# Optimization experiments

Measured on AMD Instinct MI355X. Metric: run time of the kernel, lower is better.

The kernel has to match this reference:

```python
import jax, jax.numpy as jnp
import numpy as np

K = 3  # kernel_size

def _bn(x, g, b, m, v, eps=1e-5):
    # inference-mode BatchNorm2d over channel axis 1
    sh = (1, -1, 1, 1)
    return (x - m.reshape(sh)) * (g.reshape(sh) / jnp.sqrt(v.reshape(sh) + eps)) + b.reshape(sh)

def setup_inputs() -> dict:
    key = jax.random.key(0)
    ks = jax.random.split(key, 12)
    B, C, H, W, OC = 8, 128, 96, 96, 256
    k2 = K * K
    x = jax.random.normal(ks[0], (B, C, H, W), jnp.float32)
    # get_weight grouped 1x1 conv: [C*9,1,1,1] stored compactly as [C,9]
    w1 = jax.random.normal(ks[1], (C, k2), jnp.float32) * 0.1
    # generate_feature grouped 3x3 conv (groups=C, multiplier 9): OIHW [C*9,1,3,3]
    gf_w = jax.random.normal(ks[2], (C * k2, 1, K, K), jnp.float32) * 0.1
    bn1_g = jax.random.uniform(ks[3], (C * k2,), jnp.float32, 0.5, 1.5)
    bn1_b = jax.random.normal(ks[4], (C * k2,), jnp.float32) * 0.1
    bn1_m = jax.random.normal(ks[5], (C * k2,), jnp.float32) * 0.1
    bn1_v = jax.random.uniform(ks[6], (C * k2,), jnp.float32, 0.5, 1.5)
    conv_w = jax.random.normal(ks[7], (OC, C, K, K), jnp.float32) * (1.0 / np.sqrt(C * k2))
    conv_b = jax.random.normal(ks[8], (OC,), jnp.float32) * 0.1
    bn2_g = jax.random.uniform(ks[9], (OC,), jnp.float32, 0.5, 1.5)
    bn2_b = jax.random.normal(ks[10], (OC,), jnp.float32) * 0.1
    bn2_m = jax.random.normal(ks[11], (OC,), jnp.float32) * 0.1
    bn2_v = jax.random.uniform(jax.random.fold_in(key, 99), (OC,), jnp.float32, 0.5, 1.5)
    return {"x": x, "w1": w1, "gf_w": gf_w, "bn1_g": bn1_g, "bn1_b": bn1_b,
            "bn1_m": bn1_m, "bn1_v": bn1_v, "conv_w": conv_w, "conv_b": conv_b,
            "bn2_g": bn2_g, "bn2_b": bn2_b, "bn2_m": bn2_m, "bn2_v": bn2_v}

def reference(x, w1, gf_w, bn1_g, bn1_b, bn1_m, bn1_v, conv_w, conv_b, bn2_g, bn2_b, bn2_m, bn2_v):
    B, C, H, W = x.shape
    k2 = K * K
    # --- get_weight: AvgPool2d(k=3, pad=1, stride=1, count_include_pad) + grouped 1x1 conv ---
    pooled = jax.lax.reduce_window(x, 0.0, jax.lax.add, (1, 1, K, K), (1, 1, 1, 1),
                                   [(0, 0), (0, 0), (1, 1), (1, 1)]) / float(k2)
    weight = jnp.einsum('bchw,cn->bcnhw', pooled, w1)  # [B,C,9,H,W]
    attn = jax.nn.softmax(weight, axis=2)
    # --- generate_feature: depthwise 3x3 conv (groups=C, mult 9) + BN + ReLU ---
    feat = jax.lax.conv_general_dilated(x, gf_w, (1, 1), [(1, 1), (1, 1)],
                                        dimension_numbers=('NCHW', 'OIHW', 'NCHW'),
                                        feature_group_count=C)
    feat = jax.nn.relu(_bn(feat, bn1_g, bn1_b, bn1_m, bn1_v)).reshape(B, C, k2, H, W)
    # --- attention reweight + space-to-depth rearrange 'b c (n1 n2) h w -> b c (h n1) (w n2)' ---
    wd = (feat * attn).reshape(B, C, K, K, H, W)
    wd = wd.transpose(0, 1, 4, 2, 5, 3).reshape(B, C, H * K, W * K)
    # --- final conv k=3 stride=3 + BN + ReLU ---
    out = jax.lax.conv_general_dilated(wd, conv_w, (K, K), [(0, 0), (0, 0)],
                                       dimension_numbers=('NCHW', 'OIHW', 'NCHW'))
    out = out + conv_b.reshape(1, -1, 1, 1)
    return jax.nn.relu(_bn(out, bn2_g, bn2_b, bn2_m, bn2_v))
```

## Files before the change

### kernel.cpp

```cpp
#include <hip/hip_runtime.h>
#include <hip/hip_bf16.h>


#define CCH  128
#define OCN  256
#define HH   96
#define WWD  96
#define KCH  1152
#define PIMG 9216
#define BNP  64
#define NBLK 144
#define CC   32
#define KC   288
#define VP   296
#define NT   512

using short8  = __attribute__((ext_vector_type(8))) short;
using f32x4   = __attribute__((ext_vector_type(4))) float;
using f32x2   = __attribute__((ext_vector_type(2))) float;

__device__ __forceinline__ ushort bf16bits(float f) {
    __hip_bfloat16 h = __float2bfloat16(f);
    return *reinterpret_cast<ushort*>(&h);
}

struct NB { f32x2 p[4]; float s; };

__global__ void prep_kernel(const float* __restrict__ W2, const float* __restrict__ gfw,
                            const float* __restrict__ bn1g, const float* __restrict__ bn1b,
                            const float* __restrict__ bn1m, const float* __restrict__ bn1v,
                            const float* __restrict__ w1,
                            ushort* __restrict__ W2bf, float* __restrict__ gws,
                            float* __restrict__ shiftv, float* __restrict__ w1s) {
    int i = blockIdx.x * 256 + threadIdx.x;
    if (i < OCN * KCH) {
        W2bf[i] = bf16bits(W2[i]);
    } else if (i < OCN * KCH + KCH) {
        const int ch = i - OCN * KCH;
        const float sc = bn1g[ch] * rsqrtf(bn1v[ch] + 1e-5f);
        shiftv[ch] = bn1b[ch] - bn1m[ch] * sc;
        #pragma unroll
        for (int t = 0; t < 9; ++t) gws[ch * 12 + t] = gfw[ch * 9 + t] * sc;
    } else if (i < OCN * KCH + KCH + CCH) {
        const int c = i - OCN * KCH - KCH;
        #pragma unroll
        for (int n = 0; n < 9; ++n) w1s[c * 12 + n] = w1[c * 9 + n] * (1.f / 9.f);
    }
}

__device__ __forceinline__ NB load_nb(const float* __restrict__ xc,
                                      const int hro0, const int hro1, const int hro2,
                                      const int wx0, const int wx1, const int wx2) {
    NB r;
    float v0 = xc[hro0 + wx0], v1 = xc[hro0 + wx1], v2 = xc[hro0 + wx2];
    float v3 = xc[hro1 + wx0], v4 = xc[hro1 + wx1], v5 = xc[hro1 + wx2];
    float v6 = xc[hro2 + wx0], v7 = xc[hro2 + wx1], v8 = xc[hro2 + wx2];
    r.p[0] = f32x2{v0, v1}; r.p[1] = f32x2{v2, v3};
    r.p[2] = f32x2{v4, v5}; r.p[3] = f32x2{v6, v7};
    r.s = v8;
    return r;
}

template<bool FAST>
__global__ __launch_bounds__(NT, 4) void rfa_mfma3_kernel(
    const float* __restrict__ x,
    const float* __restrict__ w1,   const float* __restrict__ gfw,
    const float* __restrict__ bn1g, const float* __restrict__ bn1b,
    const float* __restrict__ bn1m, const float* __restrict__ bn1v,
    const float* __restrict__ W2f,
    const ushort* __restrict__ W2bf, const float* __restrict__ gws,
    const float* __restrict__ shiftv, const float* __restrict__ w1s,
    const float* __restrict__ cbias,
    const float* __restrict__ bn2g, const float* __restrict__ bn2b,
    const float* __restrict__ bn2m, const float* __restrict__ bn2v,
    float* __restrict__ out)
{
    __shared__ ushort vlds[2][BNP * VP];

    const int tid = threadIdx.x;
    const int b   = blockIdx.x / NBLK;
    const int P0  = (blockIdx.x % NBLK) * BNP;

    const int px  = tid & 63;
    const int p   = P0 + px;
    const int h   = p / WWD;
    const int w   = p - h * WWD;
    const int wid = __builtin_amdgcn_readfirstlane(tid >> 6);
    const int l15 = px & 15;
    const int lhi = px >> 4;

    int hro[3], wxc[3];
    f32x2 okp[4];
    float ok8;
    {
        float okr[3], okc[3];
        #pragma unroll
        for (int d = 0; d < 3; ++d) {
            int hy = h + d - 1;
            okr[d] = ((unsigned)hy < (unsigned)HH) ? 1.f : 0.f;
            hro[d] = ((hy < 0) ? 0 : (hy > 95 ? 95 : hy)) * WWD;
            int wx = w + d - 1;
            okc[d] = ((unsigned)wx < (unsigned)WWD) ? 1.f : 0.f;
            wxc[d] = (wx < 0) ? 0 : (wx > 95 ? 95 : wx);
        }
        float o[9];
        #pragma unroll
        for (int dy = 0; dy < 3; ++dy)
            #pragma unroll
            for (int dx = 0; dx < 3; ++dx) o[dy*3+dx] = okr[dy] * okc[dx];
        okp[0] = f32x2{o[0], o[1]}; okp[1] = f32x2{o[2], o[3]};
        okp[2] = f32x2{o[4], o[5]}; okp[3] = f32x2{o[6], o[7]};
        ok8 = o[8];
    }

    f32x4 acc[2][4] = {};
    const float* xb = x + (size_t)b * CCH * PIMG;
    const int abase = (wid * 32 + l15) * KCH + lhi * 8;

    auto chan = [&](int q) { return (q >> 2) * CC + wid * 4 + (q & 3); };

    NB nb = load_nb(xb + (size_t)chan(0) * PIMG, hro[0], hro[1], hro[2], wxc[0], wxc[1], wxc[2]);

    for (int ck = 0; ck < 4; ++ck) {
        ushort* vbuf = vlds[ck & 1];

        #pragma unroll
        for (int pass = 0; pass < 4; ++pass) {
            const int q  = ck * 4 + pass;
            const int qn = (q + 1 > 15) ? 15 : q + 1;
            NB nbn = load_nb(xb + (size_t)chan(qn) * PIMG,
                             hro[0], hro[1], hro[2], wxc[0], wxc[1], wxc[2]);

            const int c  = chan(q);
            const int cl = wid * 4 + pass;
            f32x2 e[4];
            #pragma unroll
            for (int i = 0; i < 4; ++i) e[i] = nb.p[i] * okp[i];
            const float e8 = nb.s * ok8;
            f32x2 ps2 = (e[0] + e[1]) + (e[2] + e[3]);
            const float psum = ps2[0] + ps2[1] + e8;

            float at[9], ss = 0.f;
            if constexpr (FAST) {
                const float* w1r = w1s + c * 12;
                #pragma unroll
                for (int n = 0; n < 9; ++n) { at[n] = __expf(psum * w1r[n]); ss += at[n]; }
            } else {
                const float pooled = psum * (1.f / 9.f);
                const float* w1r = w1 + c * 9;
                #pragma unroll
                for (int n = 0; n < 9; ++n) { at[n] = __expf(pooled * w1r[n]); ss += at[n]; }
            }
            const float rs = __builtin_amdgcn_rcpf(ss);

            ushort* vp = vbuf + px * VP + cl * 9;
            #pragma unroll
            for (int n = 0; n < 9; ++n) {
                const int ch = c * 9 + n;
                float f;
                if constexpr (FAST) {
                    const f32x2* gp = reinterpret_cast<const f32x2*>(gws + ch * 12);
                    f32x2 f2 = f32x2{shiftv[ch], 0.f};
                    #pragma unroll
                    for (int t = 0; t < 4; ++t) f2 = __builtin_elementwise_fma(e[t], gp[t], f2);
                    f = f2[0] + f2[1];
                    f = fmaf(e8, gws[ch * 12 + 8], f);
                } else {
                    const float* gr = gfw + ch * 9;
                    float cv = 0.f;
                    cv = fmaf(e[0][0], gr[0], cv); cv = fmaf(e[0][1], gr[1], cv);
                    cv = fmaf(e[1][0], gr[2], cv); cv = fmaf(e[1][1], gr[3], cv);
                    cv = fmaf(e[2][0], gr[4], cv); cv = fmaf(e[2][1], gr[5], cv);
                    cv = fmaf(e[3][0], gr[6], cv); cv = fmaf(e[3][1], gr[7], cv);
                    cv = fmaf(e8, gr[8], cv);
                    const float sc = bn1g[ch] * rsqrtf(bn1v[ch] + 1e-5f);
                    f = (cv - bn1m[ch]) * sc + bn1b[ch];
                }
                f = fmaxf(f, 0.f) * (at[n] * rs);
                vp[n] = bf16bits(f);
            }
            nb = nbn;
        }
        __syncthreads();

        const int k0 = ck * KC;
        #pragma unroll 3
        for (int kk = 0; kk < 9; ++kk) {
            short8 afr[2], bfr[4];
            #pragma unroll
            for (int mi = 0; mi < 2; ++mi) {
                const int ai = abase + mi * 16 * KCH + k0 + kk * 32;
                if constexpr (FAST) {
                    afr[mi] = *reinterpret_cast<const short8*>(W2bf + ai);
                } else {
                    const f32x4 f0 = *reinterpret_cast<const f32x4*>(W2f + ai);
                    const f32x4 f1 = *reinterpret_cast<const f32x4*>(W2f + ai + 4);
                    short8 a;
                    a[0] = (short)bf16bits(f0[0]); a[1] = (short)bf16bits(f0[1]);
                    a[2] = (short)bf16bits(f0[2]); a[3] = (short)bf16bits(f0[3]);
                    a[4] = (short)bf16bits(f1[0]); a[5] = (short)bf16bits(f1[1]);
                    a[6] = (short)bf16bits(f1[2]); a[7] = (short)bf16bits(f1[3]);
                    afr[mi] = a;
                }
            }
            #pragma unroll
            for (int ni = 0; ni < 4; ++ni) {
                const ushort* bp = vbuf + (ni * 16 + l15) * VP + kk * 32 + lhi * 8;
                bfr[ni] = *reinterpret_cast<const short8*>(bp);
            }
            #pragma unroll
            for (int mi = 0; mi < 2; ++mi)
                #pragma unroll
                for (int ni = 0; ni < 4; ++ni)
                    acc[mi][ni] = __builtin_amdgcn_mfma_f32_16x16x32_bf16(
                        afr[mi], bfr[ni], acc[mi][ni], 0, 0, 0);
        }
    }

    #pragma unroll
    for (int mi = 0; mi < 2; ++mi) {
        #pragma unroll
        for (int r = 0; r < 4; ++r) {
            const int oc = wid * 32 + mi * 16 + lhi * 4 + r;
            const float s2 = bn2g[oc] * rsqrtf(bn2v[oc] + 1e-5f);
            const float t2 = (cbias[oc] - bn2m[oc]) * s2 + bn2b[oc];
            float* op = out + ((size_t)(b * OCN + oc)) * PIMG + P0;
            #pragma unroll
            for (int ni = 0; ni < 4; ++ni)
                op[ni * 16 + l15] = fmaxf(fmaf(acc[mi][ni][r], s2, t2), 0.f);
        }
    }
}

extern "C" void kernel_launch(void* const* d_in, const int* in_sizes, int n_in,
                              void* d_out, int out_size, void* d_ws, size_t ws_size,
                              hipStream_t stream) {
    const float* xx   = (const float*)d_in[0];
    const float* w1   = (const float*)d_in[1];
    const float* gfw  = (const float*)d_in[2];
    const float* bn1g = (const float*)d_in[3];
    const float* bn1b = (const float*)d_in[4];
    const float* bn1m = (const float*)d_in[5];
    const float* bn1v = (const float*)d_in[6];
    const float* W2   = (const float*)d_in[7];
    const float* cb   = (const float*)d_in[8];
    const float* bn2g = (const float*)d_in[9];
    const float* bn2b = (const float*)d_in[10];
    const float* bn2m = (const float*)d_in[11];
    const float* bn2v = (const float*)d_in[12];
    float* o = (float*)d_out;

    const size_t off_gws   = (size_t)OCN * KCH * sizeof(ushort);
    const size_t off_shift = off_gws + (size_t)KCH * 12 * sizeof(float);
    const size_t off_w1s   = off_shift + (size_t)KCH * sizeof(float);
    const size_t ws_need   = off_w1s + (size_t)CCH * 12 * sizeof(float);

    dim3 grid(8 * NBLK);
    dim3 blk(NT);

    if (ws_size >= ws_need) {
        ushort* W2bf = (ushort*)d_ws;
        float*  gwsp = (float*)((char*)d_ws + off_gws);
        float*  shf  = (float*)((char*)d_ws + off_shift);
        float*  w1sp = (float*)((char*)d_ws + off_w1s);
        const int ptot = OCN * KCH + KCH + CCH;
        prep_kernel<<<(ptot + 255) / 256, 256, 0, stream>>>(
            W2, gfw, bn1g, bn1b, bn1m, bn1v, w1, W2bf, gwsp, shf, w1sp);
        rfa_mfma3_kernel<true><<<grid, blk, 0, stream>>>(
            xx, w1, gfw, bn1g, bn1b, bn1m, bn1v, W2, W2bf, gwsp, shf, w1sp,
            cb, bn2g, bn2b, bn2m, bn2v, o);
    } else {
        rfa_mfma3_kernel<false><<<grid, blk, 0, stream>>>(
            xx, w1, gfw, bn1g, bn1b, bn1m, bn1v, W2, nullptr, nullptr, nullptr, nullptr,
            cb, bn2g, bn2b, bn2m, bn2v, o);
    }
}
```

Measured before the change: 210.4 us.

## Halve pixel tile per block, split channels across half-waves, use exp2

Each block now covers 32 pixels instead of 64, so the grid doubles, and the launch-bounds occupancy hint rises from 4 to 8 blocks. Each wave splits its channels between two 32-lane halves, so a pass does two channels instead of four. The software prefetch of the next channel's neighbourhood is removed. The softmax uses exp2 with log2(e) folded into the prepared weights. The aim is more parallelism and lower register pressure, at the cost of reloading the bf16 weight fragments twice as often per pixel and giving each wave half as much MFMA work per LDS stage.

```diff
diff --git a/kernel.cpp b/kernel.cpp
--- a/kernel.cpp
+++ b/kernel.cpp
@@ -8,8 +8,8 @@
 #define WWD  96
 #define KCH  1152
 #define PIMG 9216
-#define BNP  64
-#define NBLK 144
+#define BNP  32
+#define NBLK 288
 #define CC   32
 #define KC   288
 #define VP   296
@@ -23,8 +23,6 @@
     __hip_bfloat16 h = __float2bfloat16(f);
     return *reinterpret_cast<ushort*>(&h);
 }
-
-struct NB { f32x2 p[4]; float s; };
 
 __global__ void prep_kernel(const float* __restrict__ W2, const float* __restrict__ gfw,
                             const float* __restrict__ bn1g, const float* __restrict__ bn1b,
@@ -44,25 +42,13 @@
     } else if (i < OCN * KCH + KCH + CCH) {
         const int c = i - OCN * KCH - KCH;
         #pragma unroll
-        for (int n = 0; n < 9; ++n) w1s[c * 12 + n] = w1[c * 9 + n] * (1.f / 9.f);
-    }
-}
-
-__device__ __forceinline__ NB load_nb(const float* __restrict__ xc,
-                                      const int hro0, const int hro1, const int hro2,
-                                      const int wx0, const int wx1, const int wx2) {
-    NB r;
-    float v0 = xc[hro0 + wx0], v1 = xc[hro0 + wx1], v2 = xc[hro0 + wx2];
-    float v3 = xc[hro1 + wx0], v4 = xc[hro1 + wx1], v5 = xc[hro1 + wx2];
-    float v6 = xc[hro2 + wx0], v7 = xc[hro2 + wx1], v8 = xc[hro2 + wx2];
-    r.p[0] = f32x2{v0, v1}; r.p[1] = f32x2{v2, v3};
-    r.p[2] = f32x2{v4, v5}; r.p[3] = f32x2{v6, v7};
-    r.s = v8;
-    return r;
+        for (int n = 0; n < 9; ++n)
+            w1s[c * 12 + n] = w1[c * 9 + n] * (1.f / 9.f) * 1.4426950408889634f;
+    }
 }
 
 template<bool FAST>
-__global__ __launch_bounds__(NT, 4) void rfa_mfma3_kernel(
+__global__ __launch_bounds__(NT, 8) void rfa_mfma4_kernel(
     const float* __restrict__ x,
     const float* __restrict__ w1,   const float* __restrict__ gfw,
     const float* __restrict__ bn1g, const float* __restrict__ bn1b,
@@ -81,13 +67,15 @@
     const int b   = blockIdx.x / NBLK;
     const int P0  = (blockIdx.x % NBLK) * BNP;
 
-    const int px  = tid & 63;
+    const int px  = tid & 31;
+    const int cs  = (tid >> 5) & 1;
     const int p   = P0 + px;
     const int h   = p / WWD;
     const int w   = p - h * WWD;
     const int wid = __builtin_amdgcn_readfirstlane(tid >> 6);
-    const int l15 = px & 15;
-    const int lhi = px >> 4;
+    const int lane = tid & 63;
+    const int l15 = lane & 15;
+    const int lhi = lane >> 4;
 
     int hro[3], wxc[3];
     f32x2 okp[4];
@@ -103,40 +91,36 @@
             okc[d] = ((unsigned)wx < (unsigned)WWD) ? 1.f : 0.f;
             wxc[d] = (wx < 0) ? 0 : (wx > 95 ? 95 : wx);
         }
-        float o[9];
-        #pragma unroll
-        for (int dy = 0; dy < 3; ++dy)
-            #pragma unroll
-            for (int dx = 0; dx < 3; ++dx) o[dy*3+dx] = okr[dy] * okc[dx];
-        okp[0] = f32x2{o[0], o[1]}; okp[1] = f32x2{o[2], o[3]};
-        okp[2] = f32x2{o[4], o[5]}; okp[3] = f32x2{o[6], o[7]};
-        ok8 = o[8];
-    }
-
-    f32x4 acc[2][4] = {};
+        okp[0] = f32x2{okr[0]*okc[0], okr[0]*okc[1]};
+        okp[1] = f32x2{okr[0]*okc[2], okr[1]*okc[0]};
+        okp[2] = f32x2{okr[1]*okc[1], okr[1]*okc[2]};
+        okp[3] = f32x2{okr[2]*okc[0], okr[2]*okc[1]};
+        ok8    = okr[2]*okc[2];
+    }
+
+    f32x4 acc[2][2] = {};
     const float* xb = x + (size_t)b * CCH * PIMG;
     const int abase = (wid * 32 + l15) * KCH + lhi * 8;
 
-    auto chan = [&](int q) { return (q >> 2) * CC + wid * 4 + (q & 3); };
-
-    NB nb = load_nb(xb + (size_t)chan(0) * PIMG, hro[0], hro[1], hro[2], wxc[0], wxc[1], wxc[2]);
-
     for (int ck = 0; ck < 4; ++ck) {
         ushort* vbuf = vlds[ck & 1];
 
         #pragma unroll
-        for (int pass = 0; pass < 4; ++pass) {
-            const int q  = ck * 4 + pass;
-            const int qn = (q + 1 > 15) ? 15 : q + 1;
-            NB nbn = load_nb(xb + (size_t)chan(qn) * PIMG,
-                             hro[0], hro[1], hro[2], wxc[0], wxc[1], wxc[2]);
-
-            const int c  = chan(q);
-            const int cl = wid * 4 + pass;
+        for (int t = 0; t < 2; ++t) {
+            const int cl = wid * 4 + t * 2 + cs;
+            const int c  = ck * CC + cl;
+            const float* xc = xb + (size_t)c * PIMG;
+
+            const float v0 = xc[hro[0] + wxc[0]], v1 = xc[hro[0] + wxc[1]], v2 = xc[hro[0] + wxc[2]];
+            const float v3 = xc[hro[1] + wxc[0]], v4 = xc[hro[1] + wxc[1]], v5 = xc[hro[1] + wxc[2]];
+            const float v6 = xc[hro[2] + wxc[0]], v7 = xc[hro[2] + wxc[1]], v8 = xc[hro[2] + wxc[2]];
+
             f32x2 e[4];
-            #pragma unroll
-            for (int i = 0; i < 4; ++i) e[i] = nb.p[i] * okp[i];
-            const float e8 = nb.s * ok8;
+            e[0] = f32x2{v0, v1} * okp[0];
+            e[1] = f32x2{v2, v3} * okp[1];
+            e[2] = f32x2{v4, v5} * okp[2];
+            e[3] = f32x2{v6, v7} * okp[3];
+            const float e8 = v8 * ok8;
             f32x2 ps2 = (e[0] + e[1]) + (e[2] + e[3]);
             const float psum = ps2[0] + ps2[1] + e8;
 
@@ -144,7 +128,7 @@
             if constexpr (FAST) {
                 const float* w1r = w1s + c * 12;
                 #pragma unroll
-                for (int n = 0; n < 9; ++n) { at[n] = __expf(psum * w1r[n]); ss += at[n]; }
+                for (int n = 0; n < 9; ++n) { at[n] = __builtin_exp2f(psum * w1r[n]); ss += at[n]; }
             } else {
                 const float pooled = psum * (1.f / 9.f);
                 const float* w1r = w1 + c * 9;
@@ -162,7 +146,7 @@
                     const f32x2* gp = reinterpret_cast<const f32x2*>(gws + ch * 12);
                     f32x2 f2 = f32x2{shiftv[ch], 0.f};
                     #pragma unroll
-                    for (int t = 0; t < 4; ++t) f2 = __builtin_elementwise_fma(e[t], gp[t], f2);
+                    for (int u = 0; u < 4; ++u) f2 = __builtin_elementwise_fma(e[u], gp[u], f2);
                     f = f2[0] + f2[1];
                     f = fmaf(e8, gws[ch * 12 + 8], f);
                 } else {
@@ -179,14 +163,13 @@
                 f = fmaxf(f, 0.f) * (at[n] * rs);
                 vp[n] = bf16bits(f);
             }
-            nb = nbn;
         }
         __syncthreads();
 
         const int k0 = ck * KC;
         #pragma unroll 3
         for (int kk = 0; kk < 9; ++kk) {
-            short8 afr[2], bfr[4];
+            short8 afr[2], bfr[2];
             #pragma unroll
             for (int mi = 0; mi < 2; ++mi) {
                 const int ai = abase + mi * 16 * KCH + k0 + kk * 32;
@@ -204,14 +187,14 @@
                 }
             }
             #pragma unroll
-            for (int ni = 0; ni < 4; ++ni) {
+            for (int ni = 0; ni < 2; ++ni) {
                 const ushort* bp = vbuf + (ni * 16 + l15) * VP + kk * 32 + lhi * 8;
                 bfr[ni] = *reinterpret_cast<const short8*>(bp);
             }
             #pragma unroll
             for (int mi = 0; mi < 2; ++mi)
                 #pragma unroll
-                for (int ni = 0; ni < 4; ++ni)
+                for (int ni = 0; ni < 2; ++ni)
                     acc[mi][ni] = __builtin_amdgcn_mfma_f32_16x16x32_bf16(
                         afr[mi], bfr[ni], acc[mi][ni], 0, 0, 0);
         }
@@ -226,7 +209,7 @@
             const float t2 = (cbias[oc] - bn2m[oc]) * s2 + bn2b[oc];
             float* op = out + ((size_t)(b * OCN + oc)) * PIMG + P0;
             #pragma unroll
-            for (int ni = 0; ni < 4; ++ni)
+            for (int ni = 0; ni < 2; ++ni)
                 op[ni * 16 + l15] = fmaxf(fmaf(acc[mi][ni][r], s2, t2), 0.f);
         }
     }
@@ -266,11 +249,11 @@
         const int ptot = OCN * KCH + KCH + CCH;
         prep_kernel<<<(ptot + 255) / 256, 256, 0, stream>>>(
             W2, gfw, bn1g, bn1b, bn1m, bn1v, w1, W2bf, gwsp, shf, w1sp);
-        rfa_mfma3_kernel<true><<<grid, blk, 0, stream>>>(
+        rfa_mfma4_kernel<true><<<grid, blk, 0, stream>>>(
             xx, w1, gfw, bn1g, bn1b, bn1m, bn1v, W2, W2bf, gwsp, shf, w1sp,
             cb, bn2g, bn2b, bn2m, bn2v, o);
     } else {
-        rfa_mfma3_kernel<false><<<grid, blk, 0, stream>>>(
+        rfa_mfma4_kernel<false><<<grid, blk, 0, stream>>>(
             xx, w1, gfw, bn1g, bn1b, bn1m, bn1v, W2, nullptr, nullptr, nullptr, nullptr,
             cb, bn2g, bn2b, bn2m, bn2v, o);
     }
```

New measurement: 439.6 us. +108.9%, slower.
